# Kernel tuning notes

Hardware: AMD Instinct MI355X
Metric: run time of the kernel (lower is better)

Reference implementation:

```python
import jax, jax.numpy as jnp
import numpy as np

N = 50000        # nodes
E = 800000       # edges (before self-loops)
IN = 128         # in_channels
OUT = 32         # out_channels per head
H = 4            # heads
NEG_SLOPE = 0.2  # PyG GATConv leaky_relu negative slope


def setup_inputs() -> dict:
    key = jax.random.key(0)
    k1, k2, k3, k4, k5 = jax.random.split(key, 5)
    x = jax.random.normal(k1, (N, IN), dtype=jnp.float32)
    edge_index = jax.random.randint(k2, (2, E), 0, N, dtype=jnp.int32)
    # learned parameters (glorot-ish scale)
    W = jax.random.normal(k3, (H * OUT, IN), dtype=jnp.float32) * (1.0 / np.sqrt(IN))
    att_src = jax.random.normal(k4, (1, H, OUT), dtype=jnp.float32) * (1.0 / np.sqrt(OUT))
    att_dst = jax.random.normal(k5, (1, H, OUT), dtype=jnp.float32) * (1.0 / np.sqrt(OUT))
    bias = jnp.zeros((H * OUT,), dtype=jnp.float32)
    return {"x": x, "edge_index": edge_index, "W": W,
            "att_src": att_src, "att_dst": att_dst, "bias": bias}


def reference(x, edge_index, W, att_src, att_dst, bias):
    # PyG GATConv default adds self-loops
    loop = jnp.arange(N, dtype=edge_index.dtype)
    src = jnp.concatenate([edge_index[0], loop])   # [E+N]
    dst = jnp.concatenate([edge_index[1], loop])   # [E+N]

    h = (x @ W.T).reshape(N, H, OUT)               # [N,H,C]
    a_src = (h * att_src).sum(-1)                  # [N,H]
    a_dst = (h * att_dst).sum(-1)                  # [N,H]

    alpha = a_src[src] + a_dst[dst]                # [E+N,H]
    alpha = jax.nn.leaky_relu(alpha, NEG_SLOPE)

    # segment softmax over incoming edges of each destination node
    amax = jax.ops.segment_max(alpha, dst, num_segments=N)        # [N,H]
    ex = jnp.exp(alpha - amax[dst])                               # [E+N,H]
    denom = jax.ops.segment_sum(ex, dst, num_segments=N)          # [N,H]
    w = ex / denom[dst]                                           # [E+N,H]

    msg = h[src] * w[:, :, None]                                  # [E+N,H,C]
    out = jax.ops.segment_sum(msg, dst, num_segments=N)           # [N,H,C]
    return out.reshape(N, H * OUT) + bias
```

## Files before the change

kernel.cpp:

```cpp
#include <hip/hip_runtime.h>
#include <hip/hip_bf16.h>


#define IN_C  128
#define HO    128
#define NSLOPE 0.2f
#define P1_BLOCKS 256

__device__ inline unsigned pack2bf(float a, float b) {
    __hip_bfloat162 h2 = __float22bfloat162_rn(make_float2(a, b));
    unsigned r; __builtin_memcpy(&r, &h2, 4); return r;
}

__global__ __launch_bounds__(256) void k_gemm_p1(
        const float* __restrict__ x, const float* __restrict__ W,
        const float* __restrict__ att_src, const float* __restrict__ att_dst,
        unsigned* __restrict__ hb, float* __restrict__ a_src,
        float* __restrict__ a_dst, int N,
        const int* __restrict__ esrc, const int* __restrict__ edst,
        int E, int nb, int CAP,
        int* __restrict__ bucketCnt, unsigned* __restrict__ tmp) {
    __shared__ float smem[5280];
    const int t = threadIdx.x;

    if (blockIdx.x < P1_BLOCKS) {
        int* histo = (int*)smem;
        int* cur   = (int*)smem + 256;
        const int chunk = (E + P1_BLOCKS - 1) / P1_BLOCKS;
        const int beg = blockIdx.x * chunk;
        const int end = min(E, beg + chunk);
        for (int i = t; i < nb; i += 256) histo[i] = 0;
        __syncthreads();
        for (int i = beg + t; i < end; i += 256)
            atomicAdd(&histo[edst[i] >> 8], 1);
        __syncthreads();
        for (int i = t; i < nb; i += 256) {
            const int hv = histo[i];
            cur[i] = hv ? atomicAdd(&bucketCnt[i], hv) : 0;
        }
        __syncthreads();
        for (int i = beg + t; i < end; i += 256) {
            const int d = edst[i], s = esrc[i];
            const int b = d >> 8;
            const int r = atomicAdd(&cur[b], 1);
            if (r < CAP)
                tmp[(size_t)b * CAP + r] = ((unsigned)s << 8) | (unsigned)(d & 255);
        }
        return;
    }

    float (*xs)[33]   = (float(*)[33])smem;
    float (*wsT)[132] = (float(*)[132])(smem + 32 * 33);
    const int tx = t & 15, ty = t >> 4;
    const int r0 = (blockIdx.x - P1_BLOCKS) * 32;

    float acc[2][8] = {};
    const int ca = (2 * tx) ^ (((2 * tx) >> 3) & 1);
    const int cb = (2 * tx + 1) ^ (((2 * tx + 1) >> 3) & 1);

    for (int k0 = 0; k0 < IN_C; k0 += 32) {
        {
            const int row = t >> 3, cq = t & 7;
            const int gr = r0 + row;
            float4 v = make_float4(0.f, 0.f, 0.f, 0.f);
            if (gr < N) v = *(const float4*)&x[gr * IN_C + k0 + 4 * cq];
            xs[row][4 * cq + 0] = v.x; xs[row][4 * cq + 1] = v.y;
            xs[row][4 * cq + 2] = v.z; xs[row][4 * cq + 3] = v.w;
        }
        #pragma unroll
        for (int it = 0; it < 4; ++it) {
            const int s  = t + 256 * it;
            const int cl = s & 127, cq = s >> 7;
            const float4 v = *(const float4*)&W[cl * IN_C + k0 + 4 * cq];
            const int pc = (cl >> 2) ^ ((cl >> 5) & 1);
            const int pw = 4 * pc + (cl & 3);
            wsT[4 * cq + 0][pw] = v.x;
            wsT[4 * cq + 1][pw] = v.y;
            wsT[4 * cq + 2][pw] = v.z;
            wsT[4 * cq + 3][pw] = v.w;
        }
        __syncthreads();

        #pragma unroll
        for (int k = 0; k < 32; ++k) {
            const float4 wa = *(const float4*)&wsT[k][4 * ca];
            const float4 wb = *(const float4*)&wsT[k][4 * cb];
            const float x0 = xs[2 * ty + 0][k];
            const float x1 = xs[2 * ty + 1][k];
            acc[0][0] = fmaf(x0, wa.x, acc[0][0]);
            acc[0][1] = fmaf(x0, wa.y, acc[0][1]);
            acc[0][2] = fmaf(x0, wa.z, acc[0][2]);
            acc[0][3] = fmaf(x0, wa.w, acc[0][3]);
            acc[0][4] = fmaf(x0, wb.x, acc[0][4]);
            acc[0][5] = fmaf(x0, wb.y, acc[0][5]);
            acc[0][6] = fmaf(x0, wb.z, acc[0][6]);
            acc[0][7] = fmaf(x0, wb.w, acc[0][7]);
            acc[1][0] = fmaf(x1, wa.x, acc[1][0]);
            acc[1][1] = fmaf(x1, wa.y, acc[1][1]);
            acc[1][2] = fmaf(x1, wa.z, acc[1][2]);
            acc[1][3] = fmaf(x1, wa.w, acc[1][3]);
            acc[1][4] = fmaf(x1, wb.x, acc[1][4]);
            acc[1][5] = fmaf(x1, wb.y, acc[1][5]);
            acc[1][6] = fmaf(x1, wb.z, acc[1][6]);
            acc[1][7] = fmaf(x1, wb.w, acc[1][7]);
        }
        __syncthreads();
    }

    const float4 as0 = *(const float4*)&att_src[8 * tx];
    const float4 as1 = *(const float4*)&att_src[8 * tx + 4];
    const float4 ad0 = *(const float4*)&att_dst[8 * tx];
    const float4 ad1 = *(const float4*)&att_dst[8 * tx + 4];
    const int head = tx >> 2;

    #pragma unroll
    for (int i = 0; i < 2; ++i) {
        const int gr = r0 + 2 * ty + i;
        float ps = acc[i][0] * as0.x + acc[i][1] * as0.y +
                   acc[i][2] * as0.z + acc[i][3] * as0.w +
                   acc[i][4] * as1.x + acc[i][5] * as1.y +
                   acc[i][6] * as1.z + acc[i][7] * as1.w;
        float pd = acc[i][0] * ad0.x + acc[i][1] * ad0.y +
                   acc[i][2] * ad0.z + acc[i][3] * ad0.w +
                   acc[i][4] * ad1.x + acc[i][5] * ad1.y +
                   acc[i][6] * ad1.z + acc[i][7] * ad1.w;
        ps += __shfl_xor(ps, 1); ps += __shfl_xor(ps, 2);
        pd += __shfl_xor(pd, 1); pd += __shfl_xor(pd, 2);
        if (gr < N) {
            const unsigned p0 = pack2bf(acc[i][0], acc[i][1]);
            const unsigned p1 = pack2bf(acc[i][2], acc[i][3]);
            const unsigned p2 = pack2bf(acc[i][4], acc[i][5]);
            const unsigned p3 = pack2bf(acc[i][6], acc[i][7]);
            *(uint4*)&hb[gr * 64 + 4 * tx] = make_uint4(p0, p1, p2, p3);
            if ((tx & 3) == 0) {
                a_src[gr * 4 + head] = ps;
                a_dst[gr * 4 + head] = pd;
            }
        }
    }
}

__global__ __launch_bounds__(256) void p3_build(const unsigned* __restrict__ tmp,
                                                const int* __restrict__ bucketCnt,
                                                int N, int CAP, int EN,
                                                int* __restrict__ offs,
                                                int* __restrict__ col) {
    __shared__ int histo[256];
    __shared__ int cur[256];
    __shared__ int red[4];
    const int b = blockIdx.x, t = threadIdx.x;
    const int lane = t & 63, w = t >> 6;

    int part = 0;
    for (int i = t; i < b; i += 256)
        part += min(bucketCnt[i], CAP) + min(256, N - (i << 8));
    #pragma unroll
    for (int m = 1; m < 64; m <<= 1) part += __shfl_xor(part, m);
    if (lane == 0) red[w] = part;
    histo[t] = 0;
    __syncthreads();
    const int base0 = red[0] + red[1] + red[2] + red[3];

    const int d0 = b << 8;
    const int nodes = min(256, N - d0);
    const int ne = min(bucketCnt[b], CAP);
    const unsigned* tp = tmp + (size_t)b * CAP;

    for (int i = t; i < ne; i += 256)
        atomicAdd(&histo[tp[i] & 255u], 1);
    __syncthreads();

    const int v = (t < nodes) ? histo[t] + 1 : 0;
    int xsc = v;
    #pragma unroll
    for (int m = 1; m < 64; m <<= 1) {
        const int y = __shfl_up(xsc, m);
        if (lane >= m) xsc += y;
    }
    if (lane == 63) red[w] = xsc;
    __syncthreads();
    int base = base0;
    for (int j = 0; j < w; ++j) base += red[j];
    const int ex = base + xsc - v;
    if (t < nodes) {
        offs[d0 + t] = ex;
        col[ex] = d0 + t;
        cur[t] = ex + 1;
    }
    __syncthreads();
    for (int i = t; i < ne; i += 256) {
        const unsigned e = tp[i];
        col[atomicAdd(&cur[e & 255u], 1)] = (int)(e >> 8);
    }
    if (b == 0 && t == 0) offs[N] = EN;
}

__global__ __launch_bounds__(256) void k_gat(const unsigned* __restrict__ hb,
                                             const float* __restrict__ a_src,
                                             const float* __restrict__ a_dst,
                                             const int* __restrict__ offs,
                                             const int* __restrict__ col,
                                             const float* __restrict__ bias,
                                             float* __restrict__ out, int N) {
    int wid = (blockIdx.x * blockDim.x + threadIdx.x) >> 6;
    wid = __builtin_amdgcn_readfirstlane(wid);
    const int lane = threadIdx.x & 63;
    if (wid >= N) return;
    const int head = lane >> 4;
    const float ad = a_dst[wid * 4 + head];
    const float2 bv = *(const float2*)&bias[2 * lane];
    const int beg = offs[wid], end = offs[wid + 1];

    float den = 0.f, acc0 = 0.f, acc1 = 0.f;
    int e = beg;
    for (; e + 4 <= end; e += 4) {
        const int sA = col[e],     sB = col[e + 1];
        const int sC = col[e + 2], sD = col[e + 3];
        const float lsA = a_src[sA * 4 + head];
        const float lsB = a_src[sB * 4 + head];
        const float lsC = a_src[sC * 4 + head];
        const float lsD = a_src[sD * 4 + head];
        const unsigned hA = hb[sA * 64 + lane];
        const unsigned hB = hb[sB * 64 + lane];
        const unsigned hC = hb[sC * 64 + lane];
        const unsigned hD = hb[sD * 64 + lane];
        float aA = lsA + ad; aA = fmaxf(aA, NSLOPE * aA);
        float aB = lsB + ad; aB = fmaxf(aB, NSLOPE * aB);
        float aC = lsC + ad; aC = fmaxf(aC, NSLOPE * aC);
        float aD = lsD + ad; aD = fmaxf(aD, NSLOPE * aD);
        const float pA = __expf(aA), pB = __expf(aB);
        const float pC = __expf(aC), pD = __expf(aD);
        den += (pA + pB) + (pC + pD);
        acc0 = fmaf(__uint_as_float(hA << 16), pA, acc0);
        acc1 = fmaf(__uint_as_float(hA & 0xffff0000u), pA, acc1);
        acc0 = fmaf(__uint_as_float(hB << 16), pB, acc0);
        acc1 = fmaf(__uint_as_float(hB & 0xffff0000u), pB, acc1);
        acc0 = fmaf(__uint_as_float(hC << 16), pC, acc0);
        acc1 = fmaf(__uint_as_float(hC & 0xffff0000u), pC, acc1);
        acc0 = fmaf(__uint_as_float(hD << 16), pD, acc0);
        acc1 = fmaf(__uint_as_float(hD & 0xffff0000u), pD, acc1);
    }
    for (; e < end; ++e) {
        const int sA = col[e];
        const float lsA = a_src[sA * 4 + head];
        const unsigned hA = hb[sA * 64 + lane];
        float aA = lsA + ad; aA = fmaxf(aA, NSLOPE * aA);
        const float pA = __expf(aA);
        den += pA;
        acc0 = fmaf(__uint_as_float(hA << 16), pA, acc0);
        acc1 = fmaf(__uint_as_float(hA & 0xffff0000u), pA, acc1);
    }
    const float inv = 1.0f / den;
    out[wid * HO + 2 * lane]     = acc0 * inv + bv.x;
    out[wid * HO + 2 * lane + 1] = acc1 * inv + bv.y;
}

extern "C" void kernel_launch(void* const* d_in, const int* in_sizes, int n_in,
                              void* d_out, int out_size, void* d_ws, size_t ws_size,
                              hipStream_t stream) {
    const float* x       = (const float*)d_in[0];
    const int*   edge    = (const int*)d_in[1];
    const float* W       = (const float*)d_in[2];
    const float* att_src = (const float*)d_in[3];
    const float* att_dst = (const float*)d_in[4];
    const float* bias    = (const float*)d_in[5];

    const int N  = in_sizes[0] / IN_C;
    const int E  = in_sizes[1] / 2;
    const int EN = E + N;
    const int nb = (N + 255) >> 8;
    const int CAP = ((E + nb - 1) / nb) * 5 / 4 + 512;
    const int GB = (N + 31) / 32;

    char* p = (char*)d_ws;
    auto carve = [&](size_t bytes) {
        char* q = p;
        p += (bytes + 255) & ~size_t(255);
        return q;
    };
    unsigned* hb        = (unsigned*)carve((size_t)N * 64 * 4);
    float*    a_src     = (float*)carve((size_t)N * 4 * 4);
    float*    a_dst     = (float*)carve((size_t)N * 4 * 4);
    int*      offs      = (int*)carve((size_t)(N + 1) * 4);
    int*      col       = (int*)carve((size_t)EN * 4);
    int*      bucketCnt = (int*)carve(256 * 4);
    unsigned* tmp       = (unsigned*)carve((size_t)nb * CAP * 4);

    hipMemsetAsync(bucketCnt, 0, 256 * 4, stream);

    k_gemm_p1<<<P1_BLOCKS + GB, 256, 0, stream>>>(x, W, att_src, att_dst,
                                                  hb, a_src, a_dst, N,
                                                  edge, edge + E, E, nb, CAP,
                                                  bucketCnt, tmp);
    p3_build<<<nb, 256, 0, stream>>>(tmp, bucketCnt, N, CAP, EN, offs, col);
    k_gat<<<(N + 3) / 4, 256, 0, stream>>>(hb, a_src, a_dst, offs, col,
                                           bias, (float*)d_out, N);
}
```

Baseline: 100.4 us.

## Use bf16 MFMA for projection GEMM and process 4 edges per wave in aggregation

The FP32 shared-memory GEMM is replaced by a bf16 MFMA 16x16x32 path. W fragments are held in registers and each block covers 5 row tiles, with x and W rounded to bf16 before multiplication. The aggregation kernel now splits each wave into four 16-lane groups that each take every fourth edge, loading 16 bytes of features per lane, and combines the partial sums with cross-lane shuffles. An extra barrier is also added in the CSR build scan. The aim is to cut GEMM compute time and make gathers wider, at the cost of reduced GEMM input precision and 2-byte scattered stores to hb.

```diff
diff --git a/kernel.cpp b/kernel.cpp
--- a/kernel.cpp
+++ b/kernel.cpp
@@ -6,26 +6,40 @@
 #define HO    128
 #define NSLOPE 0.2f
 #define P1_BLOCKS 256
+#define ROWTILES_PER_BLOCK 5
+
+typedef __attribute__((ext_vector_type(8))) short bf16x8;
+typedef __attribute__((ext_vector_type(4))) float f32x4;
 
 __device__ inline unsigned pack2bf(float a, float b) {
     __hip_bfloat162 h2 = __float22bfloat162_rn(make_float2(a, b));
     unsigned r; __builtin_memcpy(&r, &h2, 4); return r;
 }
+__device__ inline bf16x8 pack8(float4 lo, float4 hi) {
+    union { unsigned u[4]; bf16x8 v; } r;
+    r.u[0] = pack2bf(lo.x, lo.y);
+    r.u[1] = pack2bf(lo.z, lo.w);
+    r.u[2] = pack2bf(hi.x, hi.y);
+    r.u[3] = pack2bf(hi.z, hi.w);
+    return r.v;
+}
+__device__ inline unsigned short bf16u(float a) {
+    return (unsigned short)(pack2bf(a, 0.f) & 0xffffu);
+}
 
 __global__ __launch_bounds__(256) void k_gemm_p1(
         const float* __restrict__ x, const float* __restrict__ W,
         const float* __restrict__ att_src, const float* __restrict__ att_dst,
-        unsigned* __restrict__ hb, float* __restrict__ a_src,
+        unsigned short* __restrict__ hb, float* __restrict__ a_src,
         float* __restrict__ a_dst, int N,
         const int* __restrict__ esrc, const int* __restrict__ edst,
         int E, int nb, int CAP,
         int* __restrict__ bucketCnt, unsigned* __restrict__ tmp) {
-    __shared__ float smem[5280];
     const int t = threadIdx.x;
 
     if (blockIdx.x < P1_BLOCKS) {
-        int* histo = (int*)smem;
-        int* cur   = (int*)smem + 256;
+        __shared__ int histo[256];
+        __shared__ int cur[256];
         const int chunk = (E + P1_BLOCKS - 1) / P1_BLOCKS;
         const int beg = blockIdx.x * chunk;
         const int end = min(E, beg + chunk);
@@ -49,93 +63,60 @@
         return;
     }
 
-    float (*xs)[33]   = (float(*)[33])smem;
-    float (*wsT)[132] = (float(*)[132])(smem + 32 * 33);
-    const int tx = t & 15, ty = t >> 4;
-    const int r0 = (blockIdx.x - P1_BLOCKS) * 32;
-
-    float acc[2][8] = {};
-    const int ca = (2 * tx) ^ (((2 * tx) >> 3) & 1);
-    const int cb = (2 * tx + 1) ^ (((2 * tx + 1) >> 3) & 1);
-
-    for (int k0 = 0; k0 < IN_C; k0 += 32) {
-        {
-            const int row = t >> 3, cq = t & 7;
-            const int gr = r0 + row;
-            float4 v = make_float4(0.f, 0.f, 0.f, 0.f);
-            if (gr < N) v = *(const float4*)&x[gr * IN_C + k0 + 4 * cq];
-            xs[row][4 * cq + 0] = v.x; xs[row][4 * cq + 1] = v.y;
-            xs[row][4 * cq + 2] = v.z; xs[row][4 * cq + 3] = v.w;
-        }
-        #pragma unroll
-        for (int it = 0; it < 4; ++it) {
-            const int s  = t + 256 * it;
-            const int cl = s & 127, cq = s >> 7;
-            const float4 v = *(const float4*)&W[cl * IN_C + k0 + 4 * cq];
-            const int pc = (cl >> 2) ^ ((cl >> 5) & 1);
-            const int pw = 4 * pc + (cl & 3);
-            wsT[4 * cq + 0][pw] = v.x;
-            wsT[4 * cq + 1][pw] = v.y;
-            wsT[4 * cq + 2][pw] = v.z;
-            wsT[4 * cq + 3][pw] = v.w;
-        }
-        __syncthreads();
-
-        #pragma unroll
-        for (int k = 0; k < 32; ++k) {
-            const float4 wa = *(const float4*)&wsT[k][4 * ca];
-            const float4 wb = *(const float4*)&wsT[k][4 * cb];
-            const float x0 = xs[2 * ty + 0][k];
-            const float x1 = xs[2 * ty + 1][k];
-            acc[0][0] = fmaf(x0, wa.x, acc[0][0]);
-            acc[0][1] = fmaf(x0, wa.y, acc[0][1]);
-            acc[0][2] = fmaf(x0, wa.z, acc[0][2]);
-            acc[0][3] = fmaf(x0, wa.w, acc[0][3]);
-            acc[0][4] = fmaf(x0, wb.x, acc[0][4]);
-            acc[0][5] = fmaf(x0, wb.y, acc[0][5]);
-            acc[0][6] = fmaf(x0, wb.z, acc[0][6]);
-            acc[0][7] = fmaf(x0, wb.w, acc[0][7]);
-            acc[1][0] = fmaf(x1, wa.x, acc[1][0]);
-            acc[1][1] = fmaf(x1, wa.y, acc[1][1]);
-            acc[1][2] = fmaf(x1, wa.z, acc[1][2]);
-            acc[1][3] = fmaf(x1, wa.w, acc[1][3]);
-            acc[1][4] = fmaf(x1, wb.x, acc[1][4]);
-            acc[1][5] = fmaf(x1, wb.y, acc[1][5]);
-            acc[1][6] = fmaf(x1, wb.z, acc[1][6]);
-            acc[1][7] = fmaf(x1, wb.w, acc[1][7]);
-        }
-        __syncthreads();
-    }
-
-    const float4 as0 = *(const float4*)&att_src[8 * tx];
-    const float4 as1 = *(const float4*)&att_src[8 * tx + 4];
-    const float4 ad0 = *(const float4*)&att_dst[8 * tx];
-    const float4 ad1 = *(const float4*)&att_dst[8 * tx + 4];
-    const int head = tx >> 2;
-
+    const int w    = t >> 6;
+    const int lane = t & 63;
+    const int q    = lane & 15;
+    const int kg   = lane >> 4;
+    const int col0 = 32 * w;
+
+    bf16x8 Bf[2][4];
     #pragma unroll
-    for (int i = 0; i < 2; ++i) {
-        const int gr = r0 + 2 * ty + i;
-        float ps = acc[i][0] * as0.x + acc[i][1] * as0.y +
-                   acc[i][2] * as0.z + acc[i][3] * as0.w +
-                   acc[i][4] * as1.x + acc[i][5] * as1.y +
-                   acc[i][6] * as1.z + acc[i][7] * as1.w;
-        float pd = acc[i][0] * ad0.x + acc[i][1] * ad0.y +
-                   acc[i][2] * ad0.z + acc[i][3] * ad0.w +
-                   acc[i][4] * ad1.x + acc[i][5] * ad1.y +
-                   acc[i][6] * ad1.z + acc[i][7] * ad1.w;
-        ps += __shfl_xor(ps, 1); ps += __shfl_xor(ps, 2);
-        pd += __shfl_xor(pd, 1); pd += __shfl_xor(pd, 2);
-        if (gr < N) {
-            const unsigned p0 = pack2bf(acc[i][0], acc[i][1]);
-            const unsigned p1 = pack2bf(acc[i][2], acc[i][3]);
-            const unsigned p2 = pack2bf(acc[i][4], acc[i][5]);
-            const unsigned p3 = pack2bf(acc[i][6], acc[i][7]);
-            *(uint4*)&hb[gr * 64 + 4 * tx] = make_uint4(p0, p1, p2, p3);
-            if ((tx & 3) == 0) {
-                a_src[gr * 4 + head] = ps;
-                a_dst[gr * 4 + head] = pd;
+    for (int tile = 0; tile < 2; ++tile) {
+        #pragma unroll
+        for (int c = 0; c < 4; ++c) {
+            const float* wr = W + (size_t)(col0 + 16 * tile + q) * IN_C
+                                + 32 * c + 8 * kg;
+            Bf[tile][c] = pack8(*(const float4*)wr, *(const float4*)(wr + 4));
+        }
+    }
+    const float as0 = att_src[col0 + q],      ad0 = att_dst[col0 + q];
+    const float as1 = att_src[col0 + 16 + q], ad1 = att_dst[col0 + 16 + q];
+
+    const int rowBase = (blockIdx.x - P1_BLOCKS) * (ROWTILES_PER_BLOCK * 16);
+    #pragma unroll 1
+    for (int rt = 0; rt < ROWTILES_PER_BLOCK; ++rt) {
+        const int row0 = rowBase + 16 * rt;
+        if (row0 >= N) break;
+        const float* xr = x + (size_t)(row0 + q) * IN_C + 8 * kg;
+        bf16x8 af[4];
+        #pragma unroll
+        for (int c = 0; c < 4; ++c)
+            af[c] = pack8(*(const float4*)(xr + 32 * c),
+                          *(const float4*)(xr + 32 * c + 4));
+
+        f32x4 acc0 = {0.f, 0.f, 0.f, 0.f};
+        f32x4 acc1 = {0.f, 0.f, 0.f, 0.f};
+        #pragma unroll
+        for (int c = 0; c < 4; ++c) {
+            acc0 = __builtin_amdgcn_mfma_f32_16x16x32_bf16(af[c], Bf[0][c], acc0, 0, 0, 0);
+            acc1 = __builtin_amdgcn_mfma_f32_16x16x32_bf16(af[c], Bf[1][c], acc1, 0, 0, 0);
+        }
+
+        #pragma unroll
+        for (int r = 0; r < 4; ++r) {
+            const int m = row0 + 4 * kg + r;
+            float ps = acc0[r] * as0 + acc1[r] * as1;
+            float pd = acc0[r] * ad0 + acc1[r] * ad1;
+            ps += __shfl_xor(ps, 1); ps += __shfl_xor(ps, 2);
+            ps += __shfl_xor(ps, 4); ps += __shfl_xor(ps, 8);
+            pd += __shfl_xor(pd, 1); pd += __shfl_xor(pd, 2);
+            pd += __shfl_xor(pd, 4); pd += __shfl_xor(pd, 8);
+            if (q == 0) {
+                a_src[m * 4 + w] = ps;
+                a_dst[m * 4 + w] = pd;
             }
+            hb[(size_t)m * HO + col0 + q]      = bf16u(acc0[r]);
+            hb[(size_t)m * HO + col0 + 16 + q] = bf16u(acc1[r]);
         }
     }
 }
@@ -177,6 +158,7 @@
         const int y = __shfl_up(xsc, m);
         if (lane >= m) xsc += y;
     }
+    __syncthreads();
     if (lane == 63) red[w] = xsc;
     __syncthreads();
     int base = base0;
@@ -206,53 +188,51 @@
     wid = __builtin_amdgcn_readfirstlane(wid);
     const int lane = threadIdx.x & 63;
     if (wid >= N) return;
-    const int head = lane >> 4;
+    const int g = lane >> 4, q = lane & 15;
+    const int head = q >> 2;
     const float ad = a_dst[wid * 4 + head];
-    const float2 bv = *(const float2*)&bias[2 * lane];
     const int beg = offs[wid], end = offs[wid + 1];
-
-    float den = 0.f, acc0 = 0.f, acc1 = 0.f;
-    int e = beg;
-    for (; e + 4 <= end; e += 4) {
-        const int sA = col[e],     sB = col[e + 1];
-        const int sC = col[e + 2], sD = col[e + 3];
-        const float lsA = a_src[sA * 4 + head];
-        const float lsB = a_src[sB * 4 + head];
-        const float lsC = a_src[sC * 4 + head];
-        const float lsD = a_src[sD * 4 + head];
-        const unsigned hA = hb[sA * 64 + lane];
-        const unsigned hB = hb[sB * 64 + lane];
-        const unsigned hC = hb[sC * 64 + lane];
-        const unsigned hD = hb[sD * 64 + lane];
-        float aA = lsA + ad; aA = fmaxf(aA, NSLOPE * aA);
-        float aB = lsB + ad; aB = fmaxf(aB, NSLOPE * aB);
-        float aC = lsC + ad; aC = fmaxf(aC, NSLOPE * aC);
-        float aD = lsD + ad; aD = fmaxf(aD, NSLOPE * aD);
-        const float pA = __expf(aA), pB = __expf(aB);
-        const float pC = __expf(aC), pD = __expf(aD);
-        den += (pA + pB) + (pC + pD);
-        acc0 = fmaf(__uint_as_float(hA << 16), pA, acc0);
-        acc1 = fmaf(__uint_as_float(hA & 0xffff0000u), pA, acc1);
-        acc0 = fmaf(__uint_as_float(hB << 16), pB, acc0);
-        acc1 = fmaf(__uint_as_float(hB & 0xffff0000u), pB, acc1);
-        acc0 = fmaf(__uint_as_float(hC << 16), pC, acc0);
-        acc1 = fmaf(__uint_as_float(hC & 0xffff0000u), pC, acc1);
-        acc0 = fmaf(__uint_as_float(hD << 16), pD, acc0);
-        acc1 = fmaf(__uint_as_float(hD & 0xffff0000u), pD, acc1);
-    }
-    for (; e < end; ++e) {
-        const int sA = col[e];
-        const float lsA = a_src[sA * 4 + head];
-        const unsigned hA = hb[sA * 64 + lane];
-        float aA = lsA + ad; aA = fmaxf(aA, NSLOPE * aA);
-        const float pA = __expf(aA);
-        den += pA;
-        acc0 = fmaf(__uint_as_float(hA << 16), pA, acc0);
-        acc1 = fmaf(__uint_as_float(hA & 0xffff0000u), pA, acc1);
-    }
-    const float inv = 1.0f / den;
-    out[wid * HO + 2 * lane]     = acc0 * inv + bv.x;
-    out[wid * HO + 2 * lane + 1] = acc1 * inv + bv.y;
+    const unsigned* hbq = hb + 4 * q;
+
+    float den = 0.f;
+    float a0 = 0.f, a1 = 0.f, a2 = 0.f, a3 = 0.f;
+    float a4 = 0.f, a5 = 0.f, a6 = 0.f, a7 = 0.f;
+    for (int e = beg + g; e < end; e += 4) {
+        const int s = col[e];
+        float al = a_src[s * 4 + head] + ad;
+        al = fmaxf(al, NSLOPE * al);
+        const float p = __expf(al);
+        den += p;
+        const uint4 hv = *(const uint4*)(hbq + (size_t)s * 64);
+        a0 = fmaf(__uint_as_float(hv.x << 16),          p, a0);
+        a1 = fmaf(__uint_as_float(hv.x & 0xffff0000u),  p, a1);
+        a2 = fmaf(__uint_as_float(hv.y << 16),          p, a2);
+        a3 = fmaf(__uint_as_float(hv.y & 0xffff0000u),  p, a3);
+        a4 = fmaf(__uint_as_float(hv.z << 16),          p, a4);
+        a5 = fmaf(__uint_as_float(hv.z & 0xffff0000u),  p, a5);
+        a6 = fmaf(__uint_as_float(hv.w << 16),          p, a6);
+        a7 = fmaf(__uint_as_float(hv.w & 0xffff0000u),  p, a7);
+    }
+    den += __shfl_xor(den, 16); den += __shfl_xor(den, 32);
+    a0 += __shfl_xor(a0, 16); a0 += __shfl_xor(a0, 32);
+    a1 += __shfl_xor(a1, 16); a1 += __shfl_xor(a1, 32);
+    a2 += __shfl_xor(a2, 16); a2 += __shfl_xor(a2, 32);
+    a3 += __shfl_xor(a3, 16); a3 += __shfl_xor(a3, 32);
+    a4 += __shfl_xor(a4, 16); a4 += __shfl_xor(a4, 32);
+    a5 += __shfl_xor(a5, 16); a5 += __shfl_xor(a5, 32);
+    a6 += __shfl_xor(a6, 16); a6 += __shfl_xor(a6, 32);
+    a7 += __shfl_xor(a7, 16); a7 += __shfl_xor(a7, 32);
+    if (g == 0) {
+        const float inv = 1.0f / den;
+        const float4 b0 = *(const float4*)&bias[8 * q];
+        const float4 b1 = *(const float4*)&bias[8 * q + 4];
+        float4 o0 = make_float4(fmaf(a0, inv, b0.x), fmaf(a1, inv, b0.y),
+                                fmaf(a2, inv, b0.z), fmaf(a3, inv, b0.w));
+        float4 o1 = make_float4(fmaf(a4, inv, b1.x), fmaf(a5, inv, b1.y),
+                                fmaf(a6, inv, b1.z), fmaf(a7, inv, b1.w));
+        *(float4*)&out[(size_t)wid * HO + 8 * q]     = o0;
+        *(float4*)&out[(size_t)wid * HO + 8 * q + 4] = o1;
+    }
 }
 
 extern "C" void kernel_launch(void* const* d_in, const int* in_sizes, int n_in,
@@ -270,7 +250,7 @@
     const int EN = E + N;
     const int nb = (N + 255) >> 8;
     const int CAP = ((E + nb - 1) / nb) * 5 / 4 + 512;
-    const int GB = (N + 31) / 32;
+    const int GB = (N + ROWTILES_PER_BLOCK * 16 - 1) / (ROWTILES_PER_BLOCK * 16);
 
     char* p = (char*)d_ws;
     auto carve = [&](size_t bytes) {
@@ -278,7 +258,7 @@
         p += (bytes + 255) & ~size_t(255);
         return q;
     };
-    unsigned* hb        = (unsigned*)carve((size_t)N * 64 * 4);
+    unsigned short* hb  = (unsigned short*)carve((size_t)N * HO * 2);
     float*    a_src     = (float*)carve((size_t)N * 4 * 4);
     float*    a_dst     = (float*)carve((size_t)N * 4 * 4);
     int*      offs      = (int*)carve((size_t)(N + 1) * 4);
@@ -293,6 +273,6 @@
                                                   edge, edge + E, E, nb, CAP,
                                                   bucketCnt, tmp);
     p3_build<<<nb, 256, 0, stream>>>(tmp, bucketCnt, N, CAP, EN, offs, col);
-    k_gat<<<(N + 3) / 4, 256, 0, stream>>>(hb, a_src, a_dst, offs, col,
-                                           bias, (float*)d_out, N);
-}
+    k_gat<<<(N + 3) / 4, 256, 0, stream>>>((const unsigned*)hb, a_src, a_dst,
+                                           offs, col, bias, (float*)d_out, N);
+}
```

New measurement: 92.99 us. 7.4% less time.
